# Kernel optimization log

Hardware: AMD Instinct MI355X
Metric: run time of the kernel (lower is better)

## Reference

```python
import jax, jax.numpy as jnp
import numpy as np
import math

RADIUS = 0.2
NSAMPLE = 32
M = 8
EPS = 1e-6

def _normalize(v, axis):
    n = jnp.sqrt(jnp.sum(v * v, axis=axis, keepdims=True))
    return v / (n + EPS)

def _ball_query(xyz, new_xyz, fps_idx):
    # Emulates pointnet2 ball_query: first NSAMPLE in-radius indices in scan
    # order, padded with the first found index; rows with no hits stay 0.
    B, N, _ = xyz.shape
    d2 = jnp.sum((new_xyz[:, :, None, :] - xyz[:, None, :, :]) ** 2, axis=-1)  # (B,P,N)
    mask = d2 < RADIUS * RADIUS
    keys = jnp.where(mask, jnp.arange(N, dtype=jnp.int32)[None, None, :], N)
    neg_top, _ = jax.lax.top_k(-keys, NSAMPLE)
    sorted_idx = -neg_top  # ascending first NSAMPLE in-radius indices (or N pads)
    cnt = jnp.sum(mask, axis=-1, keepdims=True)
    first = jnp.where(cnt > 0, jnp.minimum(sorted_idx[..., :1], N - 1), 0)
    j = jnp.arange(NSAMPLE)[None, None, :]
    idx = jnp.where(j < cnt, sorted_idx, first).astype(jnp.int32)
    return jnp.concatenate([fps_idx[:, :, None].astype(jnp.int32), idx], axis=-1)  # (B,P,S+1)

def _group(features, idx):
    # features (B,C,N), idx (B,P,S) -> (B,C,P,S)
    return jax.vmap(lambda f, i: f[:, i])(features, idx)

def _project_one(p):
    # reference vector in plane orthogonal to normalized p; p (B,3,P,1)
    p = _normalize(p, 1)
    px, py, pz = p[:, 0], p[:, 1], p[:, 2]
    colin = jnp.abs(px) > 1.0 - 1e-3
    rx = jnp.where(colin, -py * px, 1.0 - px * px)
    ry = jnp.where(colin, 1.0 - py * py, -px * py)
    rz = jnp.where(colin, -py * pz, -px * pz)
    return _normalize(jnp.stack([rx, ry, rz], axis=1), 1)

def _rot_sort(p, pts):
    # sort pts (B,3,P,S) along S by clockwise angle of projection onto plane orthogonal to p
    p = _normalize(p, 1)
    ref = _project_one(p)
    vert = jnp.sum(p * pts, axis=1, keepdims=True) * p
    projs = _normalize(pts - vert, 1)
    refb = jnp.broadcast_to(ref, projs.shape)
    sinus = jnp.sum(jnp.cross(refb, projs, axis=1) * p, axis=1, keepdims=True)
    cosinus = jnp.sum(refb * projs, axis=1, keepdims=True)
    angles = jnp.arctan2(sinus, cosinus)  # (B,1,P,S)
    close = jnp.sum(projs * projs, axis=1, keepdims=True) < 1e-12
    rnd = (jax.random.uniform(jax.random.key(42), angles.shape) - 0.5) * (2.0 * math.pi)
    angles = jnp.where(close, rnd, angles)
    ind = jnp.argsort(angles, axis=-1)
    return jnp.take_along_axis(pts, jnp.broadcast_to(ind, pts.shape), axis=-1)

def _calc_invariance(center, rel):
    norm2 = jnp.sqrt(jnp.sum(rel * rel, axis=1, keepdims=True) + 1e-12)
    c = _normalize(center, 1)
    cosang = jnp.sum(c * rel, axis=1, keepdims=True) / norm2
    angle = jnp.arccos(jnp.clip(cosang, -1.0 + EPS, 1.0 - EPS))
    return jnp.concatenate([norm2, angle], axis=1)  # (B,2,P,S)

def _to_quat(xyz):
    dist = jnp.sqrt(jnp.sum(xyz * xyz, axis=1, keepdims=True))
    ori = xyz / (dist + EPS)
    theta = dist / RADIUS * (math.pi / 2.0)
    return jnp.concatenate([jnp.cos(theta), jnp.sin(theta) * ori], axis=1)  # (B,4,P,S)

def _forward(xyz, new_xyz, fps_idx):
    idx = _ball_query(xyz, new_xyz, fps_idx)                 # (B,P,S+1)
    grouped = _group(jnp.swapaxes(xyz, 1, 2), idx)           # (B,3,P,S+1)
    centers = jnp.swapaxes(new_xyz, 1, 2)[..., None]         # (B,3,P,1)
    grouped = _rot_sort(centers, grouped[..., 1:] - centers) # (B,3,P,S)
    inv = _calc_invariance(centers, grouped)                 # (B,2,P,S)
    q = _to_quat(grouped)                                    # (B,4,P,S)
    quats = jnp.stack([jnp.roll(q, -m, axis=-1) for m in range(M)], axis=2)  # (B,4,M,P,S)
    B, _, _, P, S = quats.shape
    quats = quats.reshape(B, 4 * M, P, S)
    return jnp.concatenate([inv, quats], axis=1)             # (B,34,P,S)

def setup_inputs() -> dict:
    key = jax.random.key(0)
    k1, k2 = jax.random.split(key)
    B, N, P = 4, 8192, 2048
    xyz = jax.random.uniform(k1, (B, N, 3), dtype=jnp.float32)
    fps_idx = jax.random.randint(k2, (B, P), 0, N, dtype=jnp.int32)
    new_xyz = jax.vmap(lambda x, i: x[i])(xyz, fps_idx)
    return {"xyz": xyz, "new_xyz": new_xyz, "fps_idx": fps_idx}

def reference(xyz, new_xyz, fps_idx):
    return _forward(xyz, new_xyz, fps_idx)
```

## Files before the change

kernel.cpp:

```cpp
#include <hip/hip_runtime.h>
#include <math.h>


constexpr int Bc  = 4;
constexpr int Nc  = 8192;
constexpr int Pc  = 2048;
constexpr int Sc  = 32;
constexpr int CHc = 34;
constexpr int NQ  = Bc * Pc;

#define THREEFRY_PARTITIONABLE 1

#define FMUL __fmul_rn
#define FADD __fadd_rn
#define FSUB __fsub_rn

__device__ __forceinline__ unsigned tf_rotl(unsigned x, int r) {
  return (x << r) | (x >> (32 - r));
}

__device__ __forceinline__ void threefry2x32_k42(unsigned& x0, unsigned& x1) {
  const unsigned ks0 = 0u, ks1 = 42u, ks2 = 0u ^ 42u ^ 0x1BD11BDAu;
  x0 += ks0; x1 += ks1;
#define TF_ROUND(r) { x0 += x1; x1 = tf_rotl(x1, (r)); x1 ^= x0; }
  TF_ROUND(13) TF_ROUND(15) TF_ROUND(26) TF_ROUND(6)
  x0 += ks1; x1 += ks2 + 1u;
  TF_ROUND(17) TF_ROUND(29) TF_ROUND(16) TF_ROUND(24)
  x0 += ks2; x1 += ks0 + 2u;
  TF_ROUND(13) TF_ROUND(15) TF_ROUND(26) TF_ROUND(6)
  x0 += ks0; x1 += ks1 + 3u;
  TF_ROUND(17) TF_ROUND(29) TF_ROUND(16) TF_ROUND(24)
  x0 += ks1; x1 += ks2 + 4u;
  TF_ROUND(13) TF_ROUND(15) TF_ROUND(26) TF_ROUND(6)
  x0 += ks2; x1 += ks0 + 5u;
#undef TF_ROUND
}

__device__ __forceinline__ float jax_rnd_angle(unsigned n) {
#if THREEFRY_PARTITIONABLE
  unsigned x0 = 0u, x1 = n;
  threefry2x32_k42(x0, x1);
  unsigned bits = x0 ^ x1;
#else
  const unsigned half = (unsigned)(Bc * Pc * Sc) / 2u;
  unsigned x0, x1;
  bool second = (n >= half);
  if (second) { x0 = n - half; x1 = n; } else { x0 = n; x1 = n + half; }
  threefry2x32_k42(x0, x1);
  unsigned bits = second ? x1 : x0;
#endif
  float u = __uint_as_float((bits >> 9) | 0x3F800000u) - 1.0f;
  return FMUL(FSUB(u, 0.5f), (float)(2.0 * 3.141592653589793));
}

__device__ __forceinline__ float dot3rn(float ax, float ay, float az,
                                        float bx, float by, float bz) {
  return FADD(FADD(FMUL(ax, bx), FMUL(ay, by)), FMUL(az, bz));
}

__global__ __launch_bounds__(256)
void qgq_fused(const float* __restrict__ xyz,
               const float* __restrict__ new_xyz,
               float* __restrict__ out)
{
  __shared__ int sIdx[4][2 * Sc];

  const int wave = threadIdx.x >> 6;
  const int lane = threadIdx.x & 63;
  const int q0   = blockIdx.x * 8 + wave * 2;
  const int b    = q0 >> 11;
  const int p0   = q0 & 2047;

  const float* xb = xyz + (size_t)b * Nc * 3;
  const float c0x = new_xyz[((size_t)b * Pc + p0) * 3 + 0];
  const float c0y = new_xyz[((size_t)b * Pc + p0) * 3 + 1];
  const float c0z = new_xyz[((size_t)b * Pc + p0) * 3 + 2];
  const float c1x = new_xyz[((size_t)b * Pc + p0 + 1) * 3 + 0];
  const float c1y = new_xyz[((size_t)b * Pc + p0 + 1) * 3 + 1];
  const float c1z = new_xyz[((size_t)b * Pc + p0 + 1) * 3 + 2];

  int* sw = sIdx[wave];
  const float R2 = (float)(0.2 * 0.2);
  const unsigned long long below = (1ull << lane) - 1ull;

  auto loadw = [&](int basew, float xs[8], float ys[8], float zs[8]) {
    #pragma unroll
    for (int k = 0; k < 8; ++k) {
      const int i = basew + k * 64 + lane;
      xs[k] = xb[i * 3 + 0];
      ys[k] = xb[i * 3 + 1];
      zs[k] = xb[i * 3 + 2];
    }
  };

  int run0 = 0, run1 = 0;
  auto procw = [&](int basew, const float xs[8], const float ys[8],
                   const float zs[8]) {
    #pragma unroll
    for (int k = 0; k < 8; ++k) {
      const int idx = basew + k * 64 + lane;
      {
        const float dx = FSUB(c0x, xs[k]);
        const float dy = FSUB(c0y, ys[k]);
        const float dz = FSUB(c0z, zs[k]);
        const float d2 = FADD(FADD(FMUL(dx, dx), FMUL(dy, dy)), FMUL(dz, dz));
        const bool m = d2 < R2;
        const unsigned long long mask = __ballot(m);
        if (m) {
          const int pos = run0 + (int)__popcll(mask & below);
          if (pos < Sc) sw[pos] = idx;
        }
        run0 += (int)__popcll(mask);
      }
      {
        const float dx = FSUB(c1x, xs[k]);
        const float dy = FSUB(c1y, ys[k]);
        const float dz = FSUB(c1z, zs[k]);
        const float d2 = FADD(FADD(FMUL(dx, dx), FMUL(dy, dy)), FMUL(dz, dz));
        const bool m = d2 < R2;
        const unsigned long long mask = __ballot(m);
        if (m) {
          const int pos = run1 + (int)__popcll(mask & below);
          if (pos < Sc) sw[Sc + pos] = idx;
        }
        run1 += (int)__popcll(mask);
      }
    }
  };

  float ax[8], ay[8], az[8], bx[8], by[8], bz[8];
  loadw(0, ax, ay, az);
  #pragma unroll 1
  for (int basew = 0; basew < Nc; basew += 1024) {
    loadw(basew + 512, bx, by, bz);
    procw(basew, ax, ay, az);
    if (run0 >= Sc && run1 >= Sc) break;
    loadw((basew + 1024) & (Nc - 1), ax, ay, az);
    procw(basew + 512, bx, by, bz);
    if (run0 >= Sc && run1 >= Sc) break;
  }

  const int half = lane >> 5;
  const int hofs = half << 5;
  const int j    = lane & 31;
  const int q    = q0 + half;
  const int p    = q & 2047;

  const int c0c = (run0 > Sc) ? Sc : run0;
  const int c1c = (run1 > Sc) ? Sc : run1;
  const int cnt = half ? c1c : c0c;
  const float cx = half ? c1x : c0x;
  const float cy = half ? c1y : c0y;
  const float cz = half ? c1z : c0z;

  const int gi = sw[hofs + ((j < cnt) ? j : 0)];

  const float ptx = xb[gi * 3 + 0];
  const float pty = xb[gi * 3 + 1];
  const float ptz = xb[gi * 3 + 2];
  const float relx = FSUB(ptx, cx);
  const float rely = FSUB(pty, cy);
  const float relz = FSUB(ptz, cz);

  const float n1  = __fsqrt_rn(dot3rn(cx, cy, cz, cx, cy, cz));
  const float id1 = FADD(n1, 1e-6f);
  const float p1x = __fdiv_rn(cx, id1);
  const float p1y = __fdiv_rn(cy, id1);
  const float p1z = __fdiv_rn(cz, id1);

  const float n2  = __fsqrt_rn(dot3rn(p1x, p1y, p1z, p1x, p1y, p1z));
  const float id2 = FADD(n2, 1e-6f);
  const float p2x = __fdiv_rn(p1x, id2);
  const float p2y = __fdiv_rn(p1y, id2);
  const float p2z = __fdiv_rn(p1z, id2);

  const bool colin = fabsf(p2x) > (float)(1.0 - 0.001);
  const float rxv = colin ? FMUL(-p2y, p2x) : FSUB(1.0f, FMUL(p2x, p2x));
  const float ryv = colin ? FSUB(1.0f, FMUL(p2y, p2y)) : FMUL(-p2x, p2y);
  const float rzv = colin ? FMUL(-p2y, p2z) : FMUL(-p2x, p2z);
  const float nr  = __fsqrt_rn(dot3rn(rxv, ryv, rzv, rxv, ryv, rzv));
  const float idr = FADD(nr, 1e-6f);
  const float refx = __fdiv_rn(rxv, idr);
  const float refy = __fdiv_rn(ryv, idr);
  const float refz = __fdiv_rn(rzv, idr);

  const float sdot = dot3rn(p1x, p1y, p1z, relx, rely, relz);
  const float wx = FSUB(relx, FMUL(sdot, p1x));
  const float wy = FSUB(rely, FMUL(sdot, p1y));
  const float wz = FSUB(relz, FMUL(sdot, p1z));
  const float nw  = __fsqrt_rn(dot3rn(wx, wy, wz, wx, wy, wz));
  const float idw = FADD(nw, 1e-6f);
  const float prx = __fdiv_rn(wx, idw);
  const float pry = __fdiv_rn(wy, idw);
  const float prz = __fdiv_rn(wz, idw);

  const float s2 = dot3rn(prx, pry, prz, prx, pry, prz);

  float angle;
  if (s2 < 1e-12f) {
    const unsigned n = ((unsigned)q << 5) | (unsigned)j;
    angle = jax_rnd_angle(n);
  } else {
    const float ccx = FSUB(FMUL(refy, prz), FMUL(refz, pry));
    const float ccy = FSUB(FMUL(refz, prx), FMUL(refx, prz));
    const float ccz = FSUB(FMUL(refx, pry), FMUL(refy, prx));
    const float sinus   = dot3rn(ccx, ccy, ccz, p1x, p1y, p1z);
    const float cosinus = dot3rn(refx, refy, refz, prx, pry, prz);
    angle = atan2f(sinus, cosinus);
  }

  const unsigned ab   = __float_as_uint(angle);
  const unsigned skey = (ab & 0x80000000u) ? ~ab : (ab | 0x80000000u);
  unsigned long long key = ((unsigned long long)skey << 32) | (unsigned)j;

  #pragma unroll
  for (int k = 2; k <= 32; k <<= 1) {
    #pragma unroll
    for (int jj = k >> 1; jj > 0; jj >>= 1) {
      const unsigned long long other = __shfl_xor(key, jj);
      const bool up      = ((j & k) == 0);
      const bool lower   = ((j & jj) == 0);
      const bool takeMin = (lower == up);
      const unsigned long long mn = (key < other) ? key : other;
      const unsigned long long mx = (key < other) ? other : key;
      key = takeMin ? mn : mx;
    }
  }
  const int oj = (int)(key & 31u);

  const float sx = __shfl(relx, oj + hofs);
  const float sy = __shfl(rely, oj + hofs);
  const float sz = __shfl(relz, oj + hofs);

  const float dotr  = sx * sx + sy * sy + sz * sz;
  const float norm2 = sqrtf(dotr + 1e-12f);
  float cosang = (p1x * sx + p1y * sy + p1z * sz) / norm2;
  const float CL = (float)(1.0 - 1e-6);
  cosang = fminf(fmaxf(cosang, -CL), CL);
  const float ainv = acosf(cosang);

  const float dist = sqrtf(dotr);
  const float invd = 1.0f / (dist + 1e-6f);
  const float oxv = sx * invd, oyv = sy * invd, ozv = sz * invd;
  const float theta = (dist / 0.2f) * (float)(3.141592653589793 / 2.0);
  float st, ct;
  sincosf(theta, &st, &ct);
  const float qw = ct, qx = st * oxv, qy = st * oyv, qz = st * ozv;

  const size_t chs   = (size_t)Pc * Sc;
  const size_t baseo = (size_t)b * CHc * chs + (size_t)p * Sc + (size_t)j;

  out[baseo + 0 * chs] = norm2;
  out[baseo + 1 * chs] = ainv;
  #pragma unroll
  for (int m = 0; m < 8; ++m) {
    const int src = ((j + m) & 31) + hofs;
    const float vw = __shfl(qw, src);
    const float vx = __shfl(qx, src);
    const float vy = __shfl(qy, src);
    const float vz = __shfl(qz, src);
    out[baseo + (size_t)(2 + 0 * 8 + m) * chs] = vw;
    out[baseo + (size_t)(2 + 1 * 8 + m) * chs] = vx;
    out[baseo + (size_t)(2 + 2 * 8 + m) * chs] = vy;
    out[baseo + (size_t)(2 + 3 * 8 + m) * chs] = vz;
  }
}

extern "C" void kernel_launch(void* const* d_in, const int* in_sizes, int n_in,
                              void* d_out, int out_size, void* d_ws, size_t ws_size,
                              hipStream_t stream) {
  const float* xyz     = (const float*)d_in[0];
  const float* new_xyz = (const float*)d_in[1];
  float* out = (float*)d_out;

  hipLaunchKernelGGL(qgq_fused, dim3(NQ / 8), dim3(256), 0, stream,
                     xyz, new_xyz, out);
}
```

Measured before the change: 84.50 us.

## Vectorize ball-query scan with float4 loads and per-lane contiguous point chunks

The ball-query scan now gives each lane 4 contiguous points loaded as three float4 reads, replacing 24 strided scalar loads per lane. Scan order is kept by prefix-counting four ballots per center. The scan step shrinks from 512 to 256 points per iteration, so the early exit can fire at a finer granularity, but there is less load-ahead in flight to hide memory latency.

```diff
diff --git a/kernel.cpp b/kernel.cpp
--- a/kernel.cpp
+++ b/kernel.cpp
@@ -71,7 +71,9 @@
   const int b    = q0 >> 11;
   const int p0   = q0 & 2047;
 
-  const float* xb = xyz + (size_t)b * Nc * 3;
+  const float*  xb  = xyz + (size_t)b * Nc * 3;
+  const float4* xb4 = reinterpret_cast<const float4*>(xb);
+
   const float c0x = new_xyz[((size_t)b * Pc + p0) * 3 + 0];
   const float c0y = new_xyz[((size_t)b * Pc + p0) * 3 + 1];
   const float c0z = new_xyz[((size_t)b * Pc + p0) * 3 + 2];
@@ -83,61 +85,80 @@
   const float R2 = (float)(0.2 * 0.2);
   const unsigned long long below = (1ull << lane) - 1ull;
 
-  auto loadw = [&](int basew, float xs[8], float ys[8], float zs[8]) {
-    #pragma unroll
-    for (int k = 0; k < 8; ++k) {
-      const int i = basew + k * 64 + lane;
-      xs[k] = xb[i * 3 + 0];
-      ys[k] = xb[i * 3 + 1];
-      zs[k] = xb[i * 3 + 2];
+  auto loadv = [&](int basep, float4 r[3]) {
+    const float4* src = xb4 + ((basep * 3) >> 2) + 3 * lane;
+    r[0] = src[0]; r[1] = src[1]; r[2] = src[2];
+  };
+
+  int run0 = 0, run1 = 0;
+  auto procw = [&](int basep, const float4 r[3]) {
+    float px[4], py[4], pz[4];
+    px[0] = r[0].x; py[0] = r[0].y; pz[0] = r[0].z;
+    px[1] = r[0].w; py[1] = r[1].x; pz[1] = r[1].y;
+    px[2] = r[1].z; py[2] = r[1].w; pz[2] = r[2].x;
+    px[3] = r[2].y; py[3] = r[2].z; pz[3] = r[2].w;
+    const int pbase = basep + 4 * lane;
+
+    {
+      bool h[4]; unsigned long long m[4];
+      #pragma unroll
+      for (int s = 0; s < 4; ++s) {
+        const float dx = FSUB(c0x, px[s]);
+        const float dy = FSUB(c0y, py[s]);
+        const float dz = FSUB(c0z, pz[s]);
+        const float d2 = FADD(FADD(FMUL(dx, dx), FMUL(dy, dy)), FMUL(dz, dz));
+        h[s] = d2 < R2;
+        m[s] = __ballot(h[s]);
+      }
+      const int basecnt = (int)__popcll(m[0] & below) + (int)__popcll(m[1] & below)
+                        + (int)__popcll(m[2] & below) + (int)__popcll(m[3] & below);
+      int own = 0;
+      #pragma unroll
+      for (int s = 0; s < 4; ++s) {
+        if (h[s]) {
+          const int pos = run0 + basecnt + own;
+          if (pos < Sc) sw[pos] = pbase + s;
+        }
+        own += h[s] ? 1 : 0;
+      }
+      run0 += (int)__popcll(m[0]) + (int)__popcll(m[1])
+            + (int)__popcll(m[2]) + (int)__popcll(m[3]);
+    }
+    {
+      bool h[4]; unsigned long long m[4];
+      #pragma unroll
+      for (int s = 0; s < 4; ++s) {
+        const float dx = FSUB(c1x, px[s]);
+        const float dy = FSUB(c1y, py[s]);
+        const float dz = FSUB(c1z, pz[s]);
+        const float d2 = FADD(FADD(FMUL(dx, dx), FMUL(dy, dy)), FMUL(dz, dz));
+        h[s] = d2 < R2;
+        m[s] = __ballot(h[s]);
+      }
+      const int basecnt = (int)__popcll(m[0] & below) + (int)__popcll(m[1] & below)
+                        + (int)__popcll(m[2] & below) + (int)__popcll(m[3] & below);
+      int own = 0;
+      #pragma unroll
+      for (int s = 0; s < 4; ++s) {
+        if (h[s]) {
+          const int pos = run1 + basecnt + own;
+          if (pos < Sc) sw[Sc + pos] = pbase + s;
+        }
+        own += h[s] ? 1 : 0;
+      }
+      run1 += (int)__popcll(m[0]) + (int)__popcll(m[1])
+            + (int)__popcll(m[2]) + (int)__popcll(m[3]);
     }
   };
 
-  int run0 = 0, run1 = 0;
-  auto procw = [&](int basew, const float xs[8], const float ys[8],
-                   const float zs[8]) {
-    #pragma unroll
-    for (int k = 0; k < 8; ++k) {
-      const int idx = basew + k * 64 + lane;
-      {
-        const float dx = FSUB(c0x, xs[k]);
-        const float dy = FSUB(c0y, ys[k]);
-        const float dz = FSUB(c0z, zs[k]);
-        const float d2 = FADD(FADD(FMUL(dx, dx), FMUL(dy, dy)), FMUL(dz, dz));
-        const bool m = d2 < R2;
-        const unsigned long long mask = __ballot(m);
-        if (m) {
-          const int pos = run0 + (int)__popcll(mask & below);
-          if (pos < Sc) sw[pos] = idx;
-        }
-        run0 += (int)__popcll(mask);
-      }
-      {
-        const float dx = FSUB(c1x, xs[k]);
-        const float dy = FSUB(c1y, ys[k]);
-        const float dz = FSUB(c1z, zs[k]);
-        const float d2 = FADD(FADD(FMUL(dx, dx), FMUL(dy, dy)), FMUL(dz, dz));
-        const bool m = d2 < R2;
-        const unsigned long long mask = __ballot(m);
-        if (m) {
-          const int pos = run1 + (int)__popcll(mask & below);
-          if (pos < Sc) sw[Sc + pos] = idx;
-        }
-        run1 += (int)__popcll(mask);
-      }
-    }
-  };
-
-  float ax[8], ay[8], az[8], bx[8], by[8], bz[8];
-  loadw(0, ax, ay, az);
+  float4 cur[3], nxt[3];
+  loadv(0, cur);
   #pragma unroll 1
-  for (int basew = 0; basew < Nc; basew += 1024) {
-    loadw(basew + 512, bx, by, bz);
-    procw(basew, ax, ay, az);
+  for (int basep = 0; basep < Nc; basep += 256) {
+    loadv((basep + 256) & (Nc - 1), nxt);
+    procw(basep, cur);
     if (run0 >= Sc && run1 >= Sc) break;
-    loadw((basew + 1024) & (Nc - 1), ax, ay, az);
-    procw(basew + 512, bx, by, bz);
-    if (run0 >= Sc && run1 >= Sc) break;
+    cur[0] = nxt[0]; cur[1] = nxt[1]; cur[2] = nxt[2];
   }
 
   const int half = lane >> 5;
```

Result: no change. 83.44 us (-1.3%).
